# Optimization experiments

Hardware: AMD Instinct MI355X
Metric: run time of the kernel (lower is better)

Reference implementation:

```python
import jax, jax.numpy as jnp
import numpy as np

N_NODES = 50000
N_EDGES = 1250000
D_IN = 64
D_HID = 64
D_OUT = 16
N_GRAPHS = 128


def setup_inputs() -> dict:
    key = jax.random.key(0)
    ks = jax.random.split(key, 16)
    glorot = lambda k, shape: jax.random.normal(k, shape, jnp.float32) * (2.0 / (shape[0] + shape[1])) ** 0.5
    inp = {
        "x": jax.random.normal(ks[0], (N_NODES, D_IN), jnp.float32),
        "edge_index": jax.random.randint(ks[1], (2, N_EDGES), 0, N_NODES, jnp.int32),
        "adj": jnp.zeros((1,), jnp.float32),
        "batch": jnp.sort(jax.random.randint(ks[2], (N_NODES,), 0, N_GRAPHS, jnp.int32)),
        # GraphConv layer 1: lin_rel (with bias) on aggregated msgs, lin_root (no bias) on x
        "W_rel1": glorot(ks[3], (D_IN, D_HID)),
        "b_rel1": jnp.zeros((D_HID,), jnp.float32),
        "W_root1": glorot(ks[4], (D_IN, D_HID)),
        "W_rel2": glorot(ks[5], (D_HID, D_HID)),
        "b_rel2": jnp.zeros((D_HID,), jnp.float32),
        "W_root2": glorot(ks[6], (D_HID, D_HID)),
        "W_rel3": glorot(ks[7], (D_HID, D_HID)),
        "b_rel3": jnp.zeros((D_HID,), jnp.float32),
        "W_root3": glorot(ks[8], (D_HID, D_HID)),
        "W_lin": glorot(ks[9], (D_HID, D_OUT)),
        "b_lin": jnp.zeros((D_OUT,), jnp.float32),
    }
    return inp


def graph_conv(x, src, dst, W_rel, b_rel, W_root):
    # PyG GraphConv (aggr='add'): out[i] = (sum_{j->i} x[j]) @ W_rel + b_rel + x[i] @ W_root
    agg = jax.ops.segment_sum(x[src], dst, num_segments=N_NODES)  # [N, d]
    return agg @ W_rel + b_rel + x @ W_root


def reference(x, edge_index, adj, batch,
              W_rel1, b_rel1, W_root1,
              W_rel2, b_rel2, W_root2,
              W_rel3, b_rel3, W_root3,
              W_lin, b_lin):
    src, dst = edge_index[0], edge_index[1]
    h = jax.nn.relu(graph_conv(x, src, dst, W_rel1, b_rel1, W_root1))
    h = jax.nn.relu(graph_conv(h, src, dst, W_rel2, b_rel2, W_root2))
    h = graph_conv(h, src, dst, W_rel3, b_rel3, W_root3)
    # global_mean_pool over batch ids
    sums = jax.ops.segment_sum(h, batch, num_segments=N_GRAPHS)  # [G, d]
    counts = jax.ops.segment_sum(jnp.ones((h.shape[0],), h.dtype), batch, num_segments=N_GRAPHS)
    pooled = sums / jnp.maximum(counts, 1.0)[:, None]
    return pooled @ W_lin + b_lin  # [G, D_OUT]
```

## Files before the change

kernel.cpp:

```cpp
#include <hip/hip_runtime.h>

#define D 64
#define N_GRAPHS 128
#define D_OUT 16
#define BCAP 16384
#define TILE 4096
#define ECAP 2048

typedef unsigned short u16;
typedef unsigned int u32;
typedef unsigned char u8;
typedef __attribute__((ext_vector_type(8))) short bf16x8;
typedef __attribute__((ext_vector_type(4))) float f32x4;
typedef __attribute__((ext_vector_type(2))) float f32x2;

__device__ inline u16 f2bf(float f) {
  u32 u = __float_as_uint(f);
  return (u16)((u + 0x7fffu + ((u >> 16) & 1u)) >> 16);
}
__device__ inline float bf2f(u16 b) { return __uint_as_float((u32)b << 16); }
__device__ inline f32x2 bfpair(u32 v) {
  return (f32x2){__uint_as_float(v << 16), __uint_as_float(v & 0xffff0000u)};
}

__global__ __launch_bounds__(256) void cvtbin_kernel(
    const float* __restrict__ xin, u16* __restrict__ hX, int n4, int nbin,
    const int* __restrict__ src, const int* __restrict__ dst,
    int* __restrict__ cursors, u32* __restrict__ binned, int n_edges, int nbuck,
    const float* __restrict__ Wrel1, const float* __restrict__ Wroot1,
    const float* __restrict__ Wrel2, const float* __restrict__ Wroot2,
    const float* __restrict__ Wrel3, const float* __restrict__ Wroot3,
    const float* __restrict__ Wlin, const float* __restrict__ brel3,
    const float* __restrict__ blin,
    float* __restrict__ M1, float* __restrict__ M2, float* __restrict__ cvec,
    u16* __restrict__ WbT1r, u16* __restrict__ WbT1o,
    u16* __restrict__ WbT2r, u16* __restrict__ WbT2o) {
  __shared__ u32 ent[TILE];
  __shared__ u8 ebk[TILE];
  __shared__ int hist[256];
  __shared__ int startb[256];
  __shared__ int cur[256];
  __shared__ int gbase[256];
  int t = threadIdx.x;

  if ((int)blockIdx.x < nbin) {
    hist[t] = 0;
    __syncthreads();
    int base = blockIdx.x * TILE;
    int cnt = n_edges - base;
    if (cnt > TILE) cnt = TILE;

    int mys[16], myd[16];
#pragma unroll
    for (int j = 0; j < 16; j++) {
      int i = base + t + j * 256;
      if (t + j * 256 < cnt) {
        mys[j] = src[i];
        myd[j] = dst[i];
        atomicAdd(&hist[myd[j] >> 8], 1);
      } else {
        myd[j] = -1;
      }
    }
    __syncthreads();
    int myc = hist[t];
    for (int off = 1; off < 256; off <<= 1) {
      int tmp = (t >= off) ? hist[t - off] : 0;
      __syncthreads();
      hist[t] += tmp;
      __syncthreads();
    }
    int excl = hist[t] - myc;
    startb[t] = excl;
    cur[t] = excl;
    __syncthreads();

#pragma unroll
    for (int j = 0; j < 16; j++) {
      if (myd[j] >= 0) {
        int b = myd[j] >> 8;
        int p = atomicAdd(&cur[b], 1);
        ent[p] = ((u32)myd[j] << 16) | (u32)mys[j];
        ebk[p] = (u8)b;
      }
    }
    __syncthreads();

    if (t < nbuck && myc > 0) gbase[t] = atomicAdd(&cursors[t], myc);
    __syncthreads();

#pragma unroll
    for (int j = 0; j < 16; j++) {
      int p = t + j * 256;
      if (p < cnt) {
        int b = ebk[p];
        int gpos = gbase[b] + (p - startb[b]);
        if (gpos < BCAP) binned[(size_t)b * BCAP + gpos] = ent[p];
      }
    }
    return;
  }

  int cb = blockIdx.x - nbin;
  if (cb == 0) {
    if (t >= 240) {
      int o = t - 240;
      float c = blin[o];
#pragma unroll
      for (int j = 0; j < D; j++) c = fmaf(brel3[j], Wlin[j * D_OUT + o], c);
      cvec[o] = c;
    }
  } else if (cb <= 8) {
    int idx = (cb - 1) * 256 + t;
    const float* W = (idx < 1024) ? Wrel3 : Wroot3;
    float* M = (idx < 1024) ? M1 : M2;
    int id = idx & 1023;
    int k = id >> 4, o = id & 15;
    float acc = 0.0f;
#pragma unroll
    for (int j = 0; j < D; j++) acc = fmaf(W[k * D + j], Wlin[j * D_OUT + o], acc);
    M[id] = acc;
  } else if (cb <= 16) {
    int tid = (cb - 9) * 256 + t;
    int mat = tid >> 9;
    int r = tid & 511;
    int o = r >> 3;
    int k0 = (r & 7) * 8;
    const float* Wsrc = (mat == 0) ? Wrel1 : (mat == 1) ? Wroot1
                       : (mat == 2) ? Wrel2 : Wroot2;
    u16* Wdst = (mat == 0) ? WbT1r : (mat == 1) ? WbT1o
               : (mat == 2) ? WbT2r : WbT2o;
    u16 tmp[8];
#pragma unroll
    for (int j = 0; j < 8; j++) tmp[j] = f2bf(Wsrc[(k0 + j) * D + o]);
    uint4 pw;
    pw.x = (u32)tmp[0] | ((u32)tmp[1] << 16);
    pw.y = (u32)tmp[2] | ((u32)tmp[3] << 16);
    pw.z = (u32)tmp[4] | ((u32)tmp[5] << 16);
    pw.w = (u32)tmp[6] | ((u32)tmp[7] << 16);
    *(uint4*)&Wdst[o * D + k0] = pw;
  }
  int i = cb * 256 + t;
  if (i >= n4) return;
  float4 v = ((const float4*)xin)[i];
  ushort4 o4;
  o4.x = f2bf(v.x); o4.y = f2bf(v.y); o4.z = f2bf(v.z); o4.w = f2bf(v.w);
  ((ushort4*)hX)[i] = o4;
}

__global__ __launch_bounds__(256) void csr_kernel(
    const u32* __restrict__ binned, const int* __restrict__ cursors,
    u16* __restrict__ csr_src, int* __restrict__ offsets,
    int* __restrict__ midoff, int n_nodes, int nbuck, int halfThresh) {
  __shared__ int deg2[512];
  __shared__ int cur2[512];
  __shared__ int red[256];
  __shared__ u16 lcsr[BCAP];
  int b = blockIdx.x, t = threadIdx.x;
  int cnt = cursors[b];
  if (cnt < 0) cnt = 0;
  if (cnt > BCAP) cnt = BCAP;

  int c = 0;
  if (t < b) {
    c = cursors[t];
    if (c < 0) c = 0;
    if (c > BCAP) c = BCAP;
  }
  red[t] = c;
  __syncthreads();
  for (int off = 128; off > 0; off >>= 1) {
    if (t < off) red[t] += red[t + off];
    __syncthreads();
  }
  int ebase = red[0];

  int nodeBase = b << 8;
  int nn = n_nodes - nodeBase;
  if (nn > 256) nn = 256;

  deg2[t] = 0;
  deg2[t + 256] = 0;
  __syncthreads();
  const u32* be = binned + (size_t)b * BCAP;
  for (int i = t; i < cnt; i += 256) {
    u32 e = be[i];
    int ln = (e >> 16) - nodeBase;
    int half = ((int)(e & 0xffffu) >= halfThresh) ? 1 : 0;
    atomicAdd(&deg2[ln * 2 + half], 1);
  }
  __syncthreads();
  int lowc = deg2[t * 2], highc = deg2[t * 2 + 1];
  int myTotal = lowc + highc;
  red[t] = myTotal;
  __syncthreads();
  for (int off = 1; off < 256; off <<= 1) {
    int tmp = (t >= off) ? red[t - off] : 0;
    __syncthreads();
    red[t] += tmp;
    __syncthreads();
  }
  int excl = red[t] - myTotal;
  cur2[t * 2] = excl;
  cur2[t * 2 + 1] = excl + lowc;
  if (t < nn) {
    offsets[nodeBase + t] = ebase + excl;
    midoff[nodeBase + t] = ebase + excl + lowc;
  }
  if (b == nbuck - 1 && t == 0) offsets[n_nodes] = ebase + cnt;
  __syncthreads();

  for (int i = t; i < cnt; i += 256) {
    u32 e = be[i];
    int ln = (e >> 16) - nodeBase;
    int half = ((int)(e & 0xffffu) >= halfThresh) ? 1 : 0;
    int p = atomicAdd(&cur2[ln * 2 + half], 1);
    lcsr[p] = (u16)(e & 0xffffu);
  }
  __syncthreads();
  for (int i = t; i < cnt; i += 256) csr_src[ebase + i] = lcsr[i];
}

#define ACC8(a, r) \
  a[0] += bfpair(r.x); a[1] += bfpair(r.y); a[2] += bfpair(r.z); a[3] += bfpair(r.w);

#define GATHER_PROLOGUE(soff, smid, permAr, eidx, blockBase, n_nodes, offsets, midoff, csr_src, gsrc, ebase0, scnt) \
  {                                                                     \
    int t_ = threadIdx.x;                                               \
    if (t_ < 33) {                                                      \
      int idx = blockBase + t_;                                         \
      if (idx > n_nodes) idx = n_nodes;                                 \
      soff[t_] = offsets[idx];                                          \
    }                                                                   \
    if (t_ >= 64 && t_ < 96) {                                          \
      int n_ = t_ - 64;                                                 \
      int idx = blockBase + n_;                                         \
      smid[n_] = (idx < n_nodes) ? midoff[idx] : 0;                     \
    }                                                                   \
    __syncthreads();                                                    \
    ebase0 = soff[0];                                                   \
    int ecnt_ = soff[32] - ebase0;                                      \
    scnt = ecnt_ < ECAP ? ecnt_ : ECAP;                                 \
    gsrc = csr_src + ebase0;                                            \
    if (t_ < 32) {                                                      \
      int d_ = (blockBase + t_ < n_nodes) ? soff[t_ + 1] - soff[t_] : -1; \
      int r_ = 0;                                                       \
      for (int j_ = 0; j_ < 32; j_++) {                                 \
        int dj_ = (blockBase + j_ < n_nodes) ? soff[j_ + 1] - soff[j_] : -1; \
        if (dj_ > d_ || (dj_ == d_ && j_ < t_)) r_++;                   \
      }                                                                 \
      permAr[r_] = (u8)t_;                                              \
    }                                                                   \
    for (int e_ = t_; e_ < scnt; e_ += 256) eidx[e_] = gsrc[e_];        \
    __syncthreads();                                                    \
  }

#define IDX(i) ((i) < ECAP ? (int)eidx[i] : (int)gsrc[i])

#define GATHER_LOOP(h, fo, ls, le, a0, a1)                                   \
  {                                                                          \
    int i = ls;                                                              \
    for (; i + 3 < le; i += 4) {                                             \
      int s0 = IDX(i), s1 = IDX(i + 1), s2 = IDX(i + 2), s3 = IDX(i + 3);    \
      uint4 r0 = *(const uint4*)(h + ((size_t)s0 << 6) + fo);                \
      uint4 r1 = *(const uint4*)(h + ((size_t)s1 << 6) + fo);                \
      uint4 r2 = *(const uint4*)(h + ((size_t)s2 << 6) + fo);                \
      uint4 r3 = *(const uint4*)(h + ((size_t)s3 << 6) + fo);                \
      ACC8(a0, r0) ACC8(a1, r1) ACC8(a0, r2) ACC8(a1, r3)                    \
    }                                                                        \
    for (; i < le; i++) {                                                    \
      int s0 = IDX(i);                                                       \
      uint4 r0 = *(const uint4*)(h + ((size_t)s0 << 6) + fo);                \
      ACC8(a0, r0)                                                           \
    }                                                                        \
  }

__global__ __launch_bounds__(256) void fused_layer_kernel(
    const u16* __restrict__ h, const int* __restrict__ offsets,
    const int* __restrict__ midoff, const u16* __restrict__ csr_src,
    const u16* __restrict__ WbTrel, const u16* __restrict__ WbTroot,
    const float* __restrict__ brel,
    u16* __restrict__ h_out, int n_nodes, int do_relu) {
  __shared__ __align__(16) u16 ldsA[32 * 72];
  __shared__ __align__(16) u16 ldsX[32 * 72];
  __shared__ int soff[33];
  __shared__ int smid[32];
  __shared__ u8 permAr[32];
  __shared__ u16 eidx[ECAP];
  int w = threadIdx.x >> 6;
  int lane = threadIdx.x & 63;
  int sub = lane >> 3;
  int fo = (lane & 7) * 8;
  int blockBase = blockIdx.x * 32;
  const u16* gsrc;
  int ebase0, scnt;

  GATHER_PROLOGUE(soff, smid, permAr, eidx, blockBase, n_nodes, offsets, midoff, csr_src, gsrc, ebase0, scnt)

  int ln = permAr[w * 8 + sub];
  int node = blockBase + ln;
  bool valid = node < n_nodes;
  int ls = soff[ln] - ebase0;
  int le = soff[ln + 1] - ebase0;
  if (!valid) le = ls;
  int lm = valid ? smid[ln] - ebase0 : ls;
  if (lm < ls) lm = ls;
  if (lm > le) lm = le;
  int lrow = ln * 72;

  uint4 xr = make_uint4(0, 0, 0, 0);
  if (valid) xr = *(const uint4*)(h + ((size_t)node << 6) + fo);
  *(uint4*)&ldsX[lrow + fo] = xr;

  f32x2 a0[4] = {{0,0},{0,0},{0,0},{0,0}};
  f32x2 a1[4] = {{0,0},{0,0},{0,0},{0,0}};
  GATHER_LOOP(h, fo, ls, lm, a0, a1)
  GATHER_LOOP(h, fo, lm, le, a0, a1)
#pragma unroll
  for (int k = 0; k < 4; k++) a0[k] += a1[k];

  uint4 pa;
  pa.x = (u32)f2bf(a0[0].x) | ((u32)f2bf(a0[0].y) << 16);
  pa.y = (u32)f2bf(a0[1].x) | ((u32)f2bf(a0[1].y) << 16);
  pa.z = (u32)f2bf(a0[2].x) | ((u32)f2bf(a0[2].y) << 16);
  pa.w = (u32)f2bf(a0[3].x) | ((u32)f2bf(a0[3].y) << 16);
  *(uint4*)&ldsA[lrow + fo] = pa;
  __syncthreads();

  int mt = w & 1;
  int ntb = (w >> 1) * 2;
  int lr = lane & 15, lk = lane >> 4;
  int arow = (mt * 16 + lr) * 72;
  bf16x8 af0 = *(const bf16x8*)&ldsA[arow + lk * 8];
  bf16x8 af1 = *(const bf16x8*)&ldsA[arow + 32 + lk * 8];
  bf16x8 xf0 = *(const bf16x8*)&ldsX[arow + lk * 8];
  bf16x8 xf1 = *(const bf16x8*)&ldsX[arow + 32 + lk * 8];
#pragma unroll
  for (int tt = 0; tt < 2; tt++) {
    int nt = ntb + tt;
    int wrow = (nt * 16 + lr) * D + lk * 8;
    bf16x8 br0 = *(const bf16x8*)(WbTrel + wrow);
    bf16x8 br1 = *(const bf16x8*)(WbTrel + wrow + 32);
    bf16x8 bo0 = *(const bf16x8*)(WbTroot + wrow);
    bf16x8 bo1 = *(const bf16x8*)(WbTroot + wrow + 32);
    f32x4 acc = {0.0f, 0.0f, 0.0f, 0.0f};
    acc = __builtin_amdgcn_mfma_f32_16x16x32_bf16(af0, br0, acc, 0, 0, 0);
    acc = __builtin_amdgcn_mfma_f32_16x16x32_bf16(af1, br1, acc, 0, 0, 0);
    acc = __builtin_amdgcn_mfma_f32_16x16x32_bf16(xf0, bo0, acc, 0, 0, 0);
    acc = __builtin_amdgcn_mfma_f32_16x16x32_bf16(xf1, bo1, acc, 0, 0, 0);
    float bias = brel[nt * 16 + lr];
#pragma unroll
    for (int r = 0; r < 4; r++) {
      int onode = blockBase + mt * 16 + lk * 4 + r;
      if (onode < n_nodes) {
        float v = acc[r] + bias;
        if (do_relu) v = fmaxf(v, 0.0f);
        h_out[((size_t)onode << 6) + nt * 16 + lr] = f2bf(v);
      }
    }
  }
}

__global__ __launch_bounds__(256) void gather_pool_kernel(
    const u16* __restrict__ h, const int* __restrict__ offsets,
    const int* __restrict__ midoff, const u16* __restrict__ csr_src,
    const int* __restrict__ batch,
    float* __restrict__ pooledA, float* __restrict__ pooledH, int n_nodes) {
  __shared__ int soff[33];
  __shared__ int smid[32];
  __shared__ u8 permAr[32];
  __shared__ u16 eidx[ECAP];
  __shared__ int gid[32];
  __shared__ float ldsPA[32][D];
  __shared__ float ldsPH[32][D];
  int w = threadIdx.x >> 6;
  int lane = threadIdx.x & 63;
  int sub = lane >> 3;
  int fo = (lane & 7) * 8;
  int blockBase = blockIdx.x * 32;
  if (threadIdx.x < 32)
    gid[threadIdx.x] = (blockBase + threadIdx.x < n_nodes) ? batch[blockBase + threadIdx.x] : -1;
  const u16* gsrc;
  int ebase0, scnt;

  GATHER_PROLOGUE(soff, smid, permAr, eidx, blockBase, n_nodes, offsets, midoff, csr_src, gsrc, ebase0, scnt)

  int ln = permAr[w * 8 + sub];
  int node = blockBase + ln;
  bool valid = node < n_nodes;
  int ls = soff[ln] - ebase0;
  int le = soff[ln + 1] - ebase0;
  if (!valid) le = ls;
  int lm = valid ? smid[ln] - ebase0 : ls;
  if (lm < ls) lm = ls;
  if (lm > le) lm = le;

  f32x2 a0[4] = {{0,0},{0,0},{0,0},{0,0}};
  f32x2 a1[4] = {{0,0},{0,0},{0,0},{0,0}};
  GATHER_LOOP(h, fo, ls, lm, a0, a1)
  GATHER_LOOP(h, fo, lm, le, a0, a1)
#pragma unroll
  for (int k = 0; k < 4; k++) a0[k] += a1[k];

  uint4 xr = make_uint4(0, 0, 0, 0);
  if (valid) xr = *(const uint4*)(h + ((size_t)node << 6) + fo);
  f32x2 x0 = bfpair(xr.x), x1 = bfpair(xr.y), x2 = bfpair(xr.z), x3 = bfpair(xr.w);
  float* rowA = &ldsPA[ln][fo];
  float* rowH = &ldsPH[ln][fo];
  rowA[0] = a0[0].x; rowA[1] = a0[0].y; rowA[2] = a0[1].x; rowA[3] = a0[1].y;
  rowA[4] = a0[2].x; rowA[5] = a0[2].y; rowA[6] = a0[3].x; rowA[7] = a0[3].y;
  rowH[0] = x0.x; rowH[1] = x0.y; rowH[2] = x1.x; rowH[3] = x1.y;
  rowH[4] = x2.x; rowH[5] = x2.y; rowH[6] = x3.x; rowH[7] = x3.y;
  __syncthreads();

  if (threadIdx.x < 128) {
    int half = threadIdx.x >> 6;
    int f = threadIdx.x & 63;
    float* dst = half ? pooledH : pooledA;
    float acc = 0.0f;
    int curg = -1;
#pragma unroll 1
    for (int n = 0; n < 32; n++) {
      int g = gid[n];
      if (g < 0) break;
      float v = half ? ldsPH[n][f] : ldsPA[n][f];
      if (g != curg) {
        if (curg >= 0) atomicAdd(dst + curg * D + f, acc);
        curg = g;
        acc = v;
      } else {
        acc += v;
      }
    }
    if (curg >= 0) atomicAdd(dst + curg * D + f, acc);
  }
}

__global__ __launch_bounds__(64) void final_kernel(
    const float* __restrict__ pooledA, const float* __restrict__ pooledH,
    const float* __restrict__ M1, const float* __restrict__ M2,
    const float* __restrict__ cvec, const float* __restrict__ blin,
    const int* __restrict__ batch, float* __restrict__ out, int n_nodes) {
  __shared__ int seg[2];
  int g = blockIdx.x;
  int t = threadIdx.x;
  if (t < 2) {
    int target = g + t;
    int lo = 0, hi = n_nodes;
    while (lo < hi) {
      int mid = (lo + hi) >> 1;
      if (batch[mid] < target) lo = mid + 1; else hi = mid;
    }
    seg[t] = lo;
  }
  __syncthreads();
  int cnt = seg[1] - seg[0];
  if (t < D_OUT) {
    float res;
    if (cnt > 0) {
      float inv = 1.0f / (float)cnt;
      float acc = cvec[t];
#pragma unroll
      for (int k = 0; k < D; k++)
        acc = fmaf(pooledA[g * D + k] * inv, M1[k * D_OUT + t],
              fmaf(pooledH[g * D + k] * inv, M2[k * D_OUT + t], acc));
      res = acc;
    } else {
      res = blin[t];
    }
    out[g * D_OUT + t] = res;
  }
}

extern "C" void kernel_launch(void* const* d_in, const int* in_sizes, int n_in,
                              void* d_out, int out_size, void* d_ws, size_t ws_size,
                              hipStream_t stream) {
  const float* x     = (const float*)d_in[0];
  const int*   ei    = (const int*)d_in[1];
  const int*   batch = (const int*)d_in[3];
  const float* Wrel1 = (const float*)d_in[4];
  const float* brel1 = (const float*)d_in[5];
  const float* Wroot1= (const float*)d_in[6];
  const float* Wrel2 = (const float*)d_in[7];
  const float* brel2 = (const float*)d_in[8];
  const float* Wroot2= (const float*)d_in[9];
  const float* Wrel3 = (const float*)d_in[10];
  const float* brel3 = (const float*)d_in[11];
  const float* Wroot3= (const float*)d_in[12];
  const float* Wlin  = (const float*)d_in[13];
  const float* blin  = (const float*)d_in[14];
  float* out = (float*)d_out;

  const int n_edges = in_sizes[1] / 2;
  const int n_nodes = in_sizes[0] / D;
  const int* src = ei;
  const int* dst = ei + n_edges;
  const int nbuck = (n_nodes + 255) >> 8;
  const int halfThresh = n_nodes / 2;

  char* p = (char*)d_ws;
  u32* binned  = (u32*)p;    p += (size_t)nbuck * BCAP * sizeof(u32);
  int* cursors = (int*)p;    p += 256 * sizeof(int);
  float* pooledA = (float*)p; p += (size_t)N_GRAPHS * D * sizeof(float);
  float* pooledH = (float*)p; p += (size_t)N_GRAPHS * D * sizeof(float);
  float* M1     = (float*)p; p += (size_t)D * D_OUT * sizeof(float);
  float* M2     = (float*)p; p += (size_t)D * D_OUT * sizeof(float);
  float* cvec   = (float*)p; p += 16 * sizeof(float);
  int* offsets  = (int*)p;   p += (size_t)(n_nodes + 4) * sizeof(int);
  int* midoff   = (int*)p;   p += (size_t)(n_nodes + 4) * sizeof(int);
  u16* hX       = (u16*)p;   p += (size_t)n_nodes * D * sizeof(u16);
  u16* h1       = (u16*)p;   p += (size_t)n_nodes * D * sizeof(u16);
  u16* h2       = (u16*)p;   p += (size_t)n_nodes * D * sizeof(u16);
  u16* csr_src  = (u16*)p;   p += (size_t)n_edges * sizeof(u16);
  u16* WbT1r    = (u16*)p;   p += (size_t)D * D * sizeof(u16);
  u16* WbT1o    = (u16*)p;   p += (size_t)D * D * sizeof(u16);
  u16* WbT2r    = (u16*)p;   p += (size_t)D * D * sizeof(u16);
  u16* WbT2o    = (u16*)p;   p += (size_t)D * D * sizeof(u16);

  const int bin_blocks = (n_edges + TILE - 1) / TILE;
  const int cvt_n4 = n_nodes * D / 4;
  const int cvt_blocks = (cvt_n4 + 255) / 256;
  const int fused_blocks = (n_nodes + 31) / 32;

  const size_t zero_bytes = 256 * sizeof(int) + 2 * (size_t)N_GRAPHS * D * sizeof(float);
  hipMemsetAsync(cursors, 0, zero_bytes, stream);

  cvtbin_kernel<<<bin_blocks + cvt_blocks, 256, 0, stream>>>(
      x, hX, cvt_n4, bin_blocks, src, dst, cursors, binned, n_edges, nbuck,
      Wrel1, Wroot1, Wrel2, Wroot2, Wrel3, Wroot3, Wlin, brel3, blin,
      M1, M2, cvec, WbT1r, WbT1o, WbT2r, WbT2o);
  csr_kernel<<<nbuck, 256, 0, stream>>>(
      binned, cursors, csr_src, offsets, midoff, n_nodes, nbuck, halfThresh);

  fused_layer_kernel<<<fused_blocks, 256, 0, stream>>>(
      hX, offsets, midoff, csr_src, WbT1r, WbT1o, brel1, h1, n_nodes, 1);
  fused_layer_kernel<<<fused_blocks, 256, 0, stream>>>(
      h1, offsets, midoff, csr_src, WbT2r, WbT2o, brel2, h2, n_nodes, 1);

  gather_pool_kernel<<<fused_blocks, 256, 0, stream>>>(
      h2, offsets, midoff, csr_src, batch, pooledA, pooledH, n_nodes);

  final_kernel<<<N_GRAPHS, 64, 0, stream>>>(
      pooledA, pooledH, M1, M2, cvec, blin, batch, out, n_nodes);
}
```

Before: 219.3 us.

## Replace layer-3 gather with source-binned per-graph scatter pooling

Adds a second edge binning pass keyed by source node. The layer-3 aggregation-then-pool step becomes a per-source-bucket kernel: it stages h2 rows in LDS, groups edges by the destination's graph id, and accumulates into replicated pooled buffers with atomics. This replaces the per-destination gather over the CSR. The root-term pooling moves into the final kernel as a direct segment sum over h2. The cost is doubled binning work and extra workspace, and the scatter relies on 16-bit source and destination indices.

New measurement: 318.9 us. 45.4% more time.

```diff
diff --git a/kernel.cpp b/kernel.cpp
--- a/kernel.cpp
+++ b/kernel.cpp
@@ -6,6 +6,7 @@
 #define BCAP 16384
 #define TILE 4096
 #define ECAP 2048
+#define NREP 16
 
 typedef unsigned short u16;
 typedef unsigned int u32;
@@ -26,7 +27,9 @@
 __global__ __launch_bounds__(256) void cvtbin_kernel(
     const float* __restrict__ xin, u16* __restrict__ hX, int n4, int nbin,
     const int* __restrict__ src, const int* __restrict__ dst,
-    int* __restrict__ cursors, u32* __restrict__ binned, int n_edges, int nbuck,
+    int* __restrict__ cursors, u32* __restrict__ binned,
+    int* __restrict__ cursors2, u32* __restrict__ binned2,
+    int n_edges, int nbuck,
     const float* __restrict__ Wrel1, const float* __restrict__ Wroot1,
     const float* __restrict__ Wrel2, const float* __restrict__ Wroot2,
     const float* __restrict__ Wrel3, const float* __restrict__ Wroot3,
@@ -43,10 +46,17 @@
   __shared__ int gbase[256];
   int t = threadIdx.x;
 
-  if ((int)blockIdx.x < nbin) {
+  if ((int)blockIdx.x < 2 * nbin) {
+    bool bySrc = (int)blockIdx.x >= nbin;
+    const int* keyArr = bySrc ? src : dst;
+    const int* valArr = bySrc ? dst : src;
+    int* curs = bySrc ? cursors2 : cursors;
+    u32* bout = bySrc ? binned2 : binned;
+    int lb = bySrc ? (int)blockIdx.x - nbin : (int)blockIdx.x;
+
     hist[t] = 0;
     __syncthreads();
-    int base = blockIdx.x * TILE;
+    int base = lb * TILE;
     int cnt = n_edges - base;
     if (cnt > TILE) cnt = TILE;
 
@@ -55,8 +65,8 @@
     for (int j = 0; j < 16; j++) {
       int i = base + t + j * 256;
       if (t + j * 256 < cnt) {
-        mys[j] = src[i];
-        myd[j] = dst[i];
+        mys[j] = valArr[i];
+        myd[j] = keyArr[i];
         atomicAdd(&hist[myd[j] >> 8], 1);
       } else {
         myd[j] = -1;
@@ -86,7 +96,7 @@
     }
     __syncthreads();
 
-    if (t < nbuck && myc > 0) gbase[t] = atomicAdd(&cursors[t], myc);
+    if (t < nbuck && myc > 0) gbase[t] = atomicAdd(&curs[t], myc);
     __syncthreads();
 
 #pragma unroll
@@ -95,13 +105,13 @@
       if (p < cnt) {
         int b = ebk[p];
         int gpos = gbase[b] + (p - startb[b]);
-        if (gpos < BCAP) binned[(size_t)b * BCAP + gpos] = ent[p];
+        if (gpos < BCAP) bout[(size_t)b * BCAP + gpos] = ent[p];
       }
     }
     return;
   }
 
-  int cb = blockIdx.x - nbin;
+  int cb = blockIdx.x - 2 * nbin;
   if (cb == 0) {
     if (t >= 240) {
       int o = t - 240;
@@ -361,89 +371,96 @@
   }
 }
 
-__global__ __launch_bounds__(256) void gather_pool_kernel(
-    const u16* __restrict__ h, const int* __restrict__ offsets,
-    const int* __restrict__ midoff, const u16* __restrict__ csr_src,
-    const int* __restrict__ batch,
-    float* __restrict__ pooledA, float* __restrict__ pooledH, int n_nodes) {
-  __shared__ int soff[33];
-  __shared__ int smid[32];
-  __shared__ u8 permAr[32];
-  __shared__ u16 eidx[ECAP];
-  __shared__ int gid[32];
-  __shared__ float ldsPA[32][D];
-  __shared__ float ldsPH[32][D];
-  int w = threadIdx.x >> 6;
-  int lane = threadIdx.x & 63;
-  int sub = lane >> 3;
-  int fo = (lane & 7) * 8;
-  int blockBase = blockIdx.x * 32;
-  if (threadIdx.x < 32)
-    gid[threadIdx.x] = (blockBase + threadIdx.x < n_nodes) ? batch[blockBase + threadIdx.x] : -1;
-  const u16* gsrc;
-  int ebase0, scnt;
-
-  GATHER_PROLOGUE(soff, smid, permAr, eidx, blockBase, n_nodes, offsets, midoff, csr_src, gsrc, ebase0, scnt)
-
-  int ln = permAr[w * 8 + sub];
-  int node = blockBase + ln;
-  bool valid = node < n_nodes;
-  int ls = soff[ln] - ebase0;
-  int le = soff[ln + 1] - ebase0;
-  if (!valid) le = ls;
-  int lm = valid ? smid[ln] - ebase0 : ls;
-  if (lm < ls) lm = ls;
-  if (lm > le) lm = le;
-
-  f32x2 a0[4] = {{0,0},{0,0},{0,0},{0,0}};
-  f32x2 a1[4] = {{0,0},{0,0},{0,0},{0,0}};
-  GATHER_LOOP(h, fo, ls, lm, a0, a1)
-  GATHER_LOOP(h, fo, lm, le, a0, a1)
-#pragma unroll
-  for (int k = 0; k < 4; k++) a0[k] += a1[k];
-
-  uint4 xr = make_uint4(0, 0, 0, 0);
-  if (valid) xr = *(const uint4*)(h + ((size_t)node << 6) + fo);
-  f32x2 x0 = bfpair(xr.x), x1 = bfpair(xr.y), x2 = bfpair(xr.z), x3 = bfpair(xr.w);
-  float* rowA = &ldsPA[ln][fo];
-  float* rowH = &ldsPH[ln][fo];
-  rowA[0] = a0[0].x; rowA[1] = a0[0].y; rowA[2] = a0[1].x; rowA[3] = a0[1].y;
-  rowA[4] = a0[2].x; rowA[5] = a0[2].y; rowA[6] = a0[3].x; rowA[7] = a0[3].y;
-  rowH[0] = x0.x; rowH[1] = x0.y; rowH[2] = x1.x; rowH[3] = x1.y;
-  rowH[4] = x2.x; rowH[5] = x2.y; rowH[6] = x3.x; rowH[7] = x3.y;
-  __syncthreads();
-
-  if (threadIdx.x < 128) {
-    int half = threadIdx.x >> 6;
-    int f = threadIdx.x & 63;
-    float* dst = half ? pooledH : pooledA;
-    float acc = 0.0f;
-    int curg = -1;
-#pragma unroll 1
-    for (int n = 0; n < 32; n++) {
-      int g = gid[n];
-      if (g < 0) break;
-      float v = half ? ldsPH[n][f] : ldsPA[n][f];
-      if (g != curg) {
-        if (curg >= 0) atomicAdd(dst + curg * D + f, acc);
-        curg = g;
-        acc = v;
-      } else {
-        acc += v;
-      }
-    }
-    if (curg >= 0) atomicAdd(dst + curg * D + f, acc);
-  }
-}
-
-__global__ __launch_bounds__(64) void final_kernel(
-    const float* __restrict__ pooledA, const float* __restrict__ pooledH,
+__global__ __launch_bounds__(256) void pool3_kernel(
+    const u16* __restrict__ h2, const u32* __restrict__ binned2,
+    const int* __restrict__ cursors2, const int* __restrict__ batch,
+    float* __restrict__ rep, int n_nodes) {
+  __shared__ __align__(16) u16 h2lds[256 * 72];
+  __shared__ u8 sortedSrc[BCAP];
+  __shared__ int ghist[128], gcur[128], gstart[128];
+  __shared__ int red2[128];
+  int b = blockIdx.x, t = threadIdx.x;
+  int cnt = cursors2[b];
+  if (cnt < 0) cnt = 0;
+  if (cnt > BCAP) cnt = BCAP;
+  int srcBase = b << 8;
+  int nn = n_nodes - srcBase;
+  if (nn > 256) nn = 256;
+
+  for (int i = t; i < nn * 8; i += 256) {
+    int row = i >> 3, ch = i & 7;
+    *(uint4*)&h2lds[row * 72 + ch * 8] =
+        *(const uint4*)(h2 + ((size_t)(srcBase + row) << 6) + ch * 8);
+  }
+  if (t < 128) ghist[t] = 0;
+  __syncthreads();
+
+  const u32* be = binned2 + (size_t)b * BCAP;
+  for (int i = t; i < cnt; i += 256) {
+    int g = batch[be[i] & 0xffffu];
+    atomicAdd(&ghist[g], 1);
+  }
+  __syncthreads();
+  if (t < 128) red2[t] = ghist[t];
+  __syncthreads();
+  for (int off = 1; off < 128; off <<= 1) {
+    int tmp = (t >= off && t < 128) ? red2[t - off] : 0;
+    __syncthreads();
+    if (t < 128) red2[t] += tmp;
+    __syncthreads();
+  }
+  if (t < 128) {
+    gstart[t] = red2[t] - ghist[t];
+    gcur[t] = red2[t] - ghist[t];
+  }
+  __syncthreads();
+  for (int i = t; i < cnt; i += 256) {
+    u32 e = be[i];
+    int g = batch[e & 0xffffu];
+    int p = atomicAdd(&gcur[g], 1);
+    sortedSrc[p] = (u8)((e >> 16) & 0xffu);
+  }
+  __syncthreads();
+
+  int sg = t >> 3, l8 = t & 7;
+  float acc[4][8];
+#pragma unroll
+  for (int k = 0; k < 4; k++)
+#pragma unroll
+    for (int j = 0; j < 8; j++) acc[k][j] = 0.0f;
+#pragma unroll
+  for (int k = 0; k < 4; k++) {
+    int g = sg + 32 * k;
+    int s = gstart[g], e = s + ghist[g];
+    for (int i = s; i < e; i++) {
+      int sl = sortedSrc[i];
+      uint4 r = *(const uint4*)&h2lds[sl * 72 + l8 * 8];
+      f32x2 p0 = bfpair(r.x), p1 = bfpair(r.y), p2 = bfpair(r.z), p3 = bfpair(r.w);
+      acc[k][0] += p0.x; acc[k][1] += p0.y; acc[k][2] += p1.x; acc[k][3] += p1.y;
+      acc[k][4] += p2.x; acc[k][5] += p2.y; acc[k][6] += p3.x; acc[k][7] += p3.y;
+    }
+  }
+  float* myrep = rep + (size_t)(b & (NREP - 1)) * (N_GRAPHS * D);
+#pragma unroll
+  for (int k = 0; k < 4; k++) {
+    int g = sg + 32 * k;
+    if (ghist[g] > 0) {
+#pragma unroll
+      for (int j = 0; j < 8; j++)
+        atomicAdd(myrep + g * D + l8 * 8 + j, acc[k][j]);
+    }
+  }
+}
+
+__global__ __launch_bounds__(256) void final_kernel(
+    const u16* __restrict__ h2, const float* __restrict__ rep,
     const float* __restrict__ M1, const float* __restrict__ M2,
     const float* __restrict__ cvec, const float* __restrict__ blin,
     const int* __restrict__ batch, float* __restrict__ out, int n_nodes) {
   __shared__ int seg[2];
-  int g = blockIdx.x;
-  int t = threadIdx.x;
+  __shared__ float redH[256];
+  __shared__ float mA[64], mH[64];
+  int g = blockIdx.x, t = threadIdx.x;
   if (t < 2) {
     int target = g + t;
     int lo = 0, hi = n_nodes;
@@ -454,16 +471,31 @@
     seg[t] = lo;
   }
   __syncthreads();
-  int cnt = seg[1] - seg[0];
+  int start = seg[0], end = seg[1];
+  int f = t & 63, sub = t >> 6;
+  float aH = 0.0f;
+  for (int n = start + sub; n < end; n += 4)
+    aH += bf2f(h2[((size_t)n << 6) + f]);
+  redH[t] = aH;
+  __syncthreads();
+  if (t < 64) {
+    float sA = 0.0f;
+#pragma unroll
+    for (int r = 0; r < NREP; r++)
+      sA += rep[(size_t)r * (N_GRAPHS * D) + g * D + t];
+    float inv = (end > start) ? 1.0f / (float)(end - start) : 0.0f;
+    mA[t] = sA * inv;
+    mH[t] = (redH[t] + redH[64 + t] + redH[128 + t] + redH[192 + t]) * inv;
+  }
+  __syncthreads();
   if (t < D_OUT) {
     float res;
-    if (cnt > 0) {
-      float inv = 1.0f / (float)cnt;
+    if (end > start) {
       float acc = cvec[t];
 #pragma unroll
       for (int k = 0; k < D; k++)
-        acc = fmaf(pooledA[g * D + k] * inv, M1[k * D_OUT + t],
-              fmaf(pooledH[g * D + k] * inv, M2[k * D_OUT + t], acc));
+        acc = fmaf(mA[k], M1[k * D_OUT + t],
+              fmaf(mH[k], M2[k * D_OUT + t], acc));
       res = acc;
     } else {
       res = blin[t];
@@ -500,9 +532,10 @@
 
   char* p = (char*)d_ws;
   u32* binned  = (u32*)p;    p += (size_t)nbuck * BCAP * sizeof(u32);
+  u32* binned2 = (u32*)p;    p += (size_t)nbuck * BCAP * sizeof(u32);
   int* cursors = (int*)p;    p += 256 * sizeof(int);
-  float* pooledA = (float*)p; p += (size_t)N_GRAPHS * D * sizeof(float);
-  float* pooledH = (float*)p; p += (size_t)N_GRAPHS * D * sizeof(float);
+  int* cursors2= (int*)p;    p += 256 * sizeof(int);
+  float* rep   = (float*)p;  p += (size_t)NREP * N_GRAPHS * D * sizeof(float);
   float* M1     = (float*)p; p += (size_t)D * D_OUT * sizeof(float);
   float* M2     = (float*)p; p += (size_t)D * D_OUT * sizeof(float);
   float* cvec   = (float*)p; p += 16 * sizeof(float);
@@ -522,11 +555,13 @@
   const int cvt_blocks = (cvt_n4 + 255) / 256;
   const int fused_blocks = (n_nodes + 31) / 32;
 
-  const size_t zero_bytes = 256 * sizeof(int) + 2 * (size_t)N_GRAPHS * D * sizeof(float);
+  const size_t zero_bytes = 512 * sizeof(int)
+      + (size_t)NREP * N_GRAPHS * D * sizeof(float);
   hipMemsetAsync(cursors, 0, zero_bytes, stream);
 
-  cvtbin_kernel<<<bin_blocks + cvt_blocks, 256, 0, stream>>>(
-      x, hX, cvt_n4, bin_blocks, src, dst, cursors, binned, n_edges, nbuck,
+  cvtbin_kernel<<<2 * bin_blocks + cvt_blocks, 256, 0, stream>>>(
+      x, hX, cvt_n4, bin_blocks, src, dst, cursors, binned, cursors2, binned2,
+      n_edges, nbuck,
       Wrel1, Wroot1, Wrel2, Wroot2, Wrel3, Wroot3, Wlin, brel3, blin,
       M1, M2, cvec, WbT1r, WbT1o, WbT2r, WbT2o);
   csr_kernel<<<nbuck, 256, 0, stream>>>(
@@ -537,9 +572,9 @@
   fused_layer_kernel<<<fused_blocks, 256, 0, stream>>>(
       h1, offsets, midoff, csr_src, WbT2r, WbT2o, brel2, h2, n_nodes, 1);
 
-  gather_pool_kernel<<<fused_blocks, 256, 0, stream>>>(
-      h2, offsets, midoff, csr_src, batch, pooledA, pooledH, n_nodes);
-
-  final_kernel<<<N_GRAPHS, 64, 0, stream>>>(
-      pooledA, pooledH, M1, M2, cvec, blin, batch, out, n_nodes);
-}
+  pool3_kernel<<<nbuck, 256, 0, stream>>>(
+      h2, binned2, cursors2, batch, rep, n_nodes);
+
+  final_kernel<<<N_GRAPHS, 256, 0, stream>>>(
+      h2, rep, M1, M2, cvec, blin, batch, out, n_nodes);
+}
```
